# Kernel tuning notes

Hardware: AMD Instinct MI355X
Metric: run time of the kernel (lower is better)

Reference implementation:

```python
import jax, jax.numpy as jnp
import numpy as np

N, IN_F, OUT_F = 4096, 512, 256
GRAPH_DENSITY = 0.01
NEG_FILL = -1e11  # torch code uses -100000000000.0


def _normalise(g, remove_diagonal):
    # dense branch of normalise_graph (self_connection=False)
    if remove_diagonal:
        g = g - jnp.diag(jnp.diag(g))
    s = g.sum(axis=1)
    s = jnp.where(s == 0.0, 1.0, s)
    d = s ** -0.5
    return d[:, None] * g * d[None, :]


def setup_inputs() -> dict:
    key = jax.random.key(0)
    k1, k2, k3, k4, k5 = jax.random.split(key, 5)
    x = jax.random.normal(k1, (N, IN_F), jnp.float32)
    graph = (jax.random.uniform(k2, (N, N)) < GRAPH_DENSITY).astype(jnp.float32)
    # fc/weight: kaiming-normal-like init
    weight = jax.random.normal(k3, (OUT_F, IN_F), jnp.float32) * np.float32(np.sqrt(2.0 / IN_F))
    t_s = jax.random.normal(k4, (1, OUT_F), jnp.float32) * 0.05
    t_r = jax.random.normal(k5, (1, OUT_F), jnp.float32) * 0.05
    return {"x": x, "graph": graph, "weight": weight, "t_s": t_s, "t_r": t_r}


def reference(x, graph, weight, t_s, t_r):
    # H_ = input @ weight.T   (no bias, no dropout)
    H = x @ weight.T  # [N, OUT_F]

    # get_mask(graph, power=1): normalise(remove_diag) then normalise again
    mask = _normalise(_normalise(graph, remove_diagonal=True), remove_diagonal=False)  # [N, N]

    # get_edge_index_attention, dense path, attention_features == 1
    C1 = jax.nn.leaky_relu(H @ t_s.T, negative_slope=0.2)       # [N, 1]
    C2 = jax.nn.leaky_relu(H @ t_r.T, negative_slope=0.2).T    # [1, N]
    S = (mask * C1 + mask * C2) * 0.5                           # [N, N]
    S = jnp.where(mask <= 0.0, NEG_FILL, S)
    A = jax.nn.softmax(S, axis=1)                               # neighbourhood softmax

    # normalise_graph(A, remove_diagonal=False, self_connection=True), dense path
    A = A + jnp.eye(A.shape[0], dtype=A.dtype)
    s = A.sum(axis=1)
    s = jnp.where(s == 0.0, 1.0, s)
    d = s ** -0.5
    C = d[:, None] * A * d[None, :]

    return C @ H  # [N, OUT_F]
```

## Files before the change

### kernel.cpp

```cpp
#include <hip/hip_runtime.h>
#include <hip/hip_bf16.h>
#include <math.h>

#define N 4096
#define IN_F 512
#define OUT_F 256
#define CAP 128

typedef __attribute__((ext_vector_type(8))) short short8;
typedef __attribute__((ext_vector_type(4))) float float4v;

static __device__ __forceinline__ ushort f2bf(float f) {
  unsigned u = __float_as_uint(f);
  unsigned rnd = 0x7fffu + ((u >> 16) & 1u);
  return (ushort)((u + rnd) >> 16);
}

__global__ __launch_bounds__(256) void build_csr(
    const float* __restrict__ g, int* __restrict__ cols,
    int* __restrict__ deg, float* __restrict__ d1,
    float* __restrict__ c1r, float* __restrict__ c2r) {
  int i = blockIdx.x;
  __shared__ int s_cnt;
  if (threadIdx.x == 0) { s_cnt = 0; c1r[i] = 0.f; c2r[i] = 0.f; }
  __syncthreads();
  const float4* row4 = (const float4*)(g + (size_t)i * N);
  int lane = threadIdx.x & 63;
  for (int it = threadIdx.x; it < N / 4; it += 256) {
    float4 v = row4[it];
    int jb = it * 4;
    bool nz0 = (v.x != 0.f) && (jb + 0 != i);
    bool nz1 = (v.y != 0.f) && (jb + 1 != i);
    bool nz2 = (v.z != 0.f) && (jb + 2 != i);
    bool nz3 = (v.w != 0.f) && (jb + 3 != i);
    unsigned long long m0 = __ballot(nz0);
    unsigned long long m1 = __ballot(nz1);
    unsigned long long m2 = __ballot(nz2);
    unsigned long long m3 = __ballot(nz3);
    int p0 = __popcll(m0), p1 = __popcll(m1), p2 = __popcll(m2), p3 = __popcll(m3);
    int total = p0 + p1 + p2 + p3;
    if (total > 0) {
      int base;
      if (lane == 0) base = atomicAdd(&s_cnt, total);
      base = __shfl(base, 0);
      unsigned long long ltm = (1ull << lane) - 1ull;
      if (nz0) { int p = base + __popcll(m0 & ltm);                 if (p < CAP) cols[(size_t)i * CAP + p] = jb + 0; }
      if (nz1) { int p = base + p0 + __popcll(m1 & ltm);            if (p < CAP) cols[(size_t)i * CAP + p] = jb + 1; }
      if (nz2) { int p = base + p0 + p1 + __popcll(m2 & ltm);       if (p < CAP) cols[(size_t)i * CAP + p] = jb + 2; }
      if (nz3) { int p = base + p0 + p1 + p2 + __popcll(m3 & ltm);  if (p < CAP) cols[(size_t)i * CAP + p] = jb + 3; }
    }
  }
  __syncthreads();
  if (threadIdx.x == 0) {
    int c = s_cnt;
    deg[i] = (c > CAP) ? CAP : c;
    d1[i] = (c == 0) ? 1.f : rsqrtf((float)c);
  }
}

#define LDST 72
__global__ __launch_bounds__(256) void gemm_fused(
    const float* __restrict__ x, const float* __restrict__ wgt,
    const float* __restrict__ ts, const float* __restrict__ tr,
    const int* __restrict__ cols, const int* __restrict__ deg,
    const float* __restrict__ d1, float* __restrict__ w,
    float* __restrict__ H, float* __restrict__ c1r, float* __restrict__ c2r) {
  int bid = blockIdx.x;
  if (bid >= 256) {
    int i = (bid - 256) * 256 + threadIdx.x;
    int dgi = deg[i];
    float sum = 0.f;
    for (int k = 0; k < dgi; ++k) sum += d1[cols[(size_t)i * CAP + k]];
    float s2 = d1[i] * sum;
    float dd2 = (s2 == 0.f) ? 1.f : rsqrtf(s2);
    w[i] = d1[i] * dd2;
    return;
  }
  __shared__ __align__(16) ushort As[64 * LDST];
  __shared__ __align__(16) ushort Bs[64 * LDST];
  int bm = (bid >> 2) * 64;
  int bn = (bid & 3) * 64;
  int tid = threadIdx.x;
  int lane = tid & 63;
  int wv = tid >> 6;
  int wm = (wv >> 1) * 32, wn = (wv & 1) * 32;

  float4v acc[2][2] = {{{0.f,0.f,0.f,0.f},{0.f,0.f,0.f,0.f}},
                       {{0.f,0.f,0.f,0.f},{0.f,0.f,0.f,0.f}}};

  for (int k0 = 0; k0 < IN_F; k0 += 64) {
    #pragma unroll
    for (int p = 0; p < 4; ++p) {
      int idx = p * 256 + tid;
      int row = idx >> 4;
      int cg = idx & 15;
      float4 va = *(const float4*)(x   + (size_t)(bm + row) * IN_F + k0 + cg * 4);
      float4 vb = *(const float4*)(wgt + (size_t)(bn + row) * IN_F + k0 + cg * 4);
      ushort4 pa, pb;
      pa.x = f2bf(va.x); pa.y = f2bf(va.y); pa.z = f2bf(va.z); pa.w = f2bf(va.w);
      pb.x = f2bf(vb.x); pb.y = f2bf(vb.y); pb.z = f2bf(vb.z); pb.w = f2bf(vb.w);
      *(ushort4*)(As + row * LDST + cg * 4) = pa;
      *(ushort4*)(Bs + row * LDST + cg * 4) = pb;
    }
    __syncthreads();
    #pragma unroll
    for (int kk = 0; kk < 64; kk += 32) {
      int kof = kk + (lane >> 4) * 8;
      short8 a0 = *(const short8*)(As + (wm +      (lane & 15)) * LDST + kof);
      short8 a1 = *(const short8*)(As + (wm + 16 + (lane & 15)) * LDST + kof);
      short8 b0 = *(const short8*)(Bs + (wn +      (lane & 15)) * LDST + kof);
      short8 b1 = *(const short8*)(Bs + (wn + 16 + (lane & 15)) * LDST + kof);
      acc[0][0] = __builtin_amdgcn_mfma_f32_16x16x32_bf16(a0, b0, acc[0][0], 0, 0, 0);
      acc[0][1] = __builtin_amdgcn_mfma_f32_16x16x32_bf16(a0, b1, acc[0][1], 0, 0, 0);
      acc[1][0] = __builtin_amdgcn_mfma_f32_16x16x32_bf16(a1, b0, acc[1][0], 0, 0, 0);
      acc[1][1] = __builtin_amdgcn_mfma_f32_16x16x32_bf16(a1, b1, acc[1][1], 0, 0, 0);
    }
    __syncthreads();
  }
  int ccol = lane & 15;
  int crow = (lane >> 4) * 4;
  float ts0 = ts[bn + wn + ccol],      ts1 = ts[bn + wn + 16 + ccol];
  float tr0 = tr[bn + wn + ccol],      tr1 = tr[bn + wn + 16 + ccol];
  #pragma unroll
  for (int rt = 0; rt < 2; ++rt) {
    #pragma unroll
    for (int r = 0; r < 4; ++r) {
      float ps = acc[rt][0][r] * ts0 + acc[rt][1][r] * ts1;
      float pr = acc[rt][0][r] * tr0 + acc[rt][1][r] * tr1;
      #pragma unroll
      for (int off = 1; off < 16; off <<= 1) {
        ps += __shfl_xor(ps, off);
        pr += __shfl_xor(pr, off);
      }
      if (ccol == 0) {
        int row = bm + wm + rt * 16 + crow + r;
        atomicAdd(&c1r[row], ps);
        atomicAdd(&c2r[row], pr);
      }
    }
  }
  #pragma unroll
  for (int rt = 0; rt < 2; ++rt)
    #pragma unroll
    for (int ct = 0; ct < 2; ++ct)
      #pragma unroll
      for (int r = 0; r < 4; ++r) {
        int gr = bm + wm + rt * 16 + crow + r;
        int gc = bn + wn + ct * 16 + ccol;
        H[(size_t)gr * OUT_F + gc] = acc[rt][ct][r];
      }
}

__global__ __launch_bounds__(256) void aggregate(
    const float* __restrict__ H, const int* __restrict__ cols,
    const int* __restrict__ deg, const float* __restrict__ w,
    const float* __restrict__ c1r, const float* __restrict__ c2r,
    float* __restrict__ out) {
  __shared__ int sJ[4][CAP];
  __shared__ float sA[4][CAP];
  int wv = threadIdx.x >> 6;
  int lane = threadIdx.x & 63;
  int i = blockIdx.x * 4 + wv;
  int dgi = deg[i];
  float wi = w[i];
  float c1v = c1r[i];
  float ci = c1v > 0.f ? c1v : 0.2f * c1v;

  float S0 = -1e30f, S1 = -1e30f;
  int j0 = 0, j1 = 0;
  if (lane < dgi) {
    j0 = cols[(size_t)i * CAP + lane];
    float c2v = c2r[j0];
    float cj = c2v > 0.f ? c2v : 0.2f * c2v;
    S0 = 0.5f * wi * w[j0] * (ci + cj);
  }
  if (lane + 64 < dgi) {
    j1 = cols[(size_t)i * CAP + lane + 64];
    float c2v = c2r[j1];
    float cj = c2v > 0.f ? c2v : 0.2f * c2v;
    S1 = 0.5f * wi * w[j1] * (ci + cj);
  }
  float mx = fmaxf(S0, S1);
  #pragma unroll
  for (int off = 32; off > 0; off >>= 1) mx = fmaxf(mx, __shfl_xor(mx, off));
  float e0 = (lane < dgi) ? __expf(S0 - mx) : 0.f;
  float e1 = (lane + 64 < dgi) ? __expf(S1 - mx) : 0.f;
  float Z = e0 + e1;
  #pragma unroll
  for (int off = 32; off > 0; off >>= 1) Z += __shfl_xor(Z, off);
  float half_invZ = 0.5f / Z;
  if (lane < dgi)      { sJ[wv][lane] = j0;        sA[wv][lane] = e0 * half_invZ; }
  if (lane + 64 < dgi) { sJ[wv][lane + 64] = j1;   sA[wv][lane + 64] = e1 * half_invZ; }
  __syncthreads();

  float4 hself = ((const float4*)(H + (size_t)i * OUT_F))[lane];
  float4 accv;
  accv.x = 0.5f * hself.x; accv.y = 0.5f * hself.y;
  accv.z = 0.5f * hself.z; accv.w = 0.5f * hself.w;

  if (dgi > 0) {
    int k = 0;
    for (; k + 8 <= dgi; k += 8) {
      int jj[8]; float aa[8];
      #pragma unroll
      for (int u = 0; u < 8; ++u) { jj[u] = sJ[wv][k + u]; aa[u] = sA[wv][k + u]; }
      float4 h[8];
      #pragma unroll
      for (int u = 0; u < 8; ++u)
        h[u] = ((const float4*)(H + (size_t)jj[u] * OUT_F))[lane];
      #pragma unroll
      for (int u = 0; u < 8; ++u) {
        accv.x += aa[u] * h[u].x;
        accv.y += aa[u] * h[u].y;
        accv.z += aa[u] * h[u].z;
        accv.w += aa[u] * h[u].w;
      }
    }
    for (; k < dgi; ++k) {
      int ja = sJ[wv][k];
      float aa = sA[wv][k];
      float4 ha = ((const float4*)(H + (size_t)ja * OUT_F))[lane];
      accv.x += aa * ha.x; accv.y += aa * ha.y;
      accv.z += aa * ha.z; accv.w += aa * ha.w;
    }
  } else {
    float4 s = {0.f, 0.f, 0.f, 0.f};
    for (int r = 0; r < N; ++r) {
      float4 h = ((const float4*)(H + (size_t)r * OUT_F))[lane];
      s.x += h.x; s.y += h.y; s.z += h.z; s.w += h.w;
    }
    const float inv = 0.5f / (float)N;
    accv.x += s.x * inv; accv.y += s.y * inv;
    accv.z += s.z * inv; accv.w += s.w * inv;
  }
  ((float4*)(out + (size_t)i * OUT_F))[lane] = accv;
}

extern "C" void kernel_launch(void* const* d_in, const int* in_sizes, int n_in,
                              void* d_out, int out_size, void* d_ws, size_t ws_size,
                              hipStream_t stream) {
  const float* x     = (const float*)d_in[0];
  const float* graph = (const float*)d_in[1];
  const float* wgt   = (const float*)d_in[2];
  const float* ts    = (const float*)d_in[3];
  const float* tr    = (const float*)d_in[4];
  float* out = (float*)d_out;

  char* ws = (char*)d_ws;
  float* H    = (float*)(ws);
  int*   cols = (int*)  (ws + (size_t)4 * 1024 * 1024);
  int*   deg  = (int*)  (ws + (size_t)6 * 1024 * 1024);
  float* d1   = (float*)(ws + (size_t)6 * 1024 * 1024 + 16384);
  float* w    = (float*)(ws + (size_t)6 * 1024 * 1024 + 32768);
  float* c1r  = (float*)(ws + (size_t)6 * 1024 * 1024 + 49152);
  float* c2r  = (float*)(ws + (size_t)6 * 1024 * 1024 + 65536);

  build_csr<<<N, 256, 0, stream>>>(graph, cols, deg, d1, c1r, c2r);
  gemm_fused<<<272, 256, 0, stream>>>(x, wgt, ts, tr, cols, deg, d1, w, H, c1r, c2r);
  aggregate<<<N / 4, 256, 0, stream>>>(H, cols, deg, w, c1r, c2r, out);
}
```

Before: 138.6 us.

## Gather neighbour rows from a bf16 copy of H and compute C1 in aggregate

The GEMM now also writes a bf16 copy of H, and the aggregate kernel gathers neighbour rows from it, halving the bytes per gathered row. The per-row C1 score is now taken in aggregate as a dot of the row's own H with t_s, which removes the C1 atomics from the GEMM epilogue. The per-row degree normalisation is reworked from one thread per row with a serial loop into a wave-per-row reduction, using 320 blocks. A block-wide __syncthreads in aggregate is dropped because each wave only reads its own shared slots, and bf16 H lowers the precision of the aggregation.

```diff
diff --git a/kernel.cpp b/kernel.cpp
--- a/kernel.cpp
+++ b/kernel.cpp
@@ -15,14 +15,16 @@
   unsigned rnd = 0x7fffu + ((u >> 16) & 1u);
   return (ushort)((u + rnd) >> 16);
 }
+static __device__ __forceinline__ float bf2f(ushort us) {
+  return __uint_as_float(((unsigned)us) << 16);
+}
 
 __global__ __launch_bounds__(256) void build_csr(
     const float* __restrict__ g, int* __restrict__ cols,
-    int* __restrict__ deg, float* __restrict__ d1,
-    float* __restrict__ c1r, float* __restrict__ c2r) {
+    int* __restrict__ deg, float* __restrict__ d1, float* __restrict__ c2r) {
   int i = blockIdx.x;
   __shared__ int s_cnt;
-  if (threadIdx.x == 0) { s_cnt = 0; c1r[i] = 0.f; c2r[i] = 0.f; }
+  if (threadIdx.x == 0) { s_cnt = 0; c2r[i] = 0.f; }
   __syncthreads();
   const float4* row4 = (const float4*)(g + (size_t)i * N);
   int lane = threadIdx.x & 63;
@@ -61,19 +63,27 @@
 #define LDST 72
 __global__ __launch_bounds__(256) void gemm_fused(
     const float* __restrict__ x, const float* __restrict__ wgt,
-    const float* __restrict__ ts, const float* __restrict__ tr,
+    const float* __restrict__ tr,
     const int* __restrict__ cols, const int* __restrict__ deg,
     const float* __restrict__ d1, float* __restrict__ w,
-    float* __restrict__ H, float* __restrict__ c1r, float* __restrict__ c2r) {
+    float* __restrict__ H, ushort* __restrict__ Hb, float* __restrict__ c2r) {
   int bid = blockIdx.x;
   if (bid >= 256) {
-    int i = (bid - 256) * 256 + threadIdx.x;
-    int dgi = deg[i];
-    float sum = 0.f;
-    for (int k = 0; k < dgi; ++k) sum += d1[cols[(size_t)i * CAP + k]];
-    float s2 = d1[i] * sum;
-    float dd2 = (s2 == 0.f) ? 1.f : rsqrtf(s2);
-    w[i] = d1[i] * dd2;
+    int wv = threadIdx.x >> 6, lane = threadIdx.x & 63;
+    int wave_id = (bid - 256) * 4 + wv;
+    for (int r = 0; r < 16; ++r) {
+      int i = wave_id * 16 + r;
+      int dgi = deg[i];
+      float v = 0.f;
+      if (lane < dgi)      v  = d1[cols[(size_t)i * CAP + lane]];
+      if (lane + 64 < dgi) v += d1[cols[(size_t)i * CAP + lane + 64]];
+      #pragma unroll
+      for (int off = 32; off > 0; off >>= 1) v += __shfl_xor(v, off);
+      if (lane == 0) {
+        float s2 = d1[i] * v;
+        w[i] = d1[i] * ((s2 == 0.f) ? 1.f : rsqrtf(s2));
+      }
+    }
     return;
   }
   __shared__ __align__(16) ushort As[64 * LDST];
@@ -119,22 +129,16 @@
   }
   int ccol = lane & 15;
   int crow = (lane >> 4) * 4;
-  float ts0 = ts[bn + wn + ccol],      ts1 = ts[bn + wn + 16 + ccol];
-  float tr0 = tr[bn + wn + ccol],      tr1 = tr[bn + wn + 16 + ccol];
+  float tr0 = tr[bn + wn + ccol], tr1 = tr[bn + wn + 16 + ccol];
   #pragma unroll
   for (int rt = 0; rt < 2; ++rt) {
     #pragma unroll
     for (int r = 0; r < 4; ++r) {
-      float ps = acc[rt][0][r] * ts0 + acc[rt][1][r] * ts1;
       float pr = acc[rt][0][r] * tr0 + acc[rt][1][r] * tr1;
       #pragma unroll
-      for (int off = 1; off < 16; off <<= 1) {
-        ps += __shfl_xor(ps, off);
-        pr += __shfl_xor(pr, off);
-      }
+      for (int off = 1; off < 16; off <<= 1) pr += __shfl_xor(pr, off);
       if (ccol == 0) {
         int row = bm + wm + rt * 16 + crow + r;
-        atomicAdd(&c1r[row], ps);
         atomicAdd(&c2r[row], pr);
       }
     }
@@ -147,15 +151,17 @@
       for (int r = 0; r < 4; ++r) {
         int gr = bm + wm + rt * 16 + crow + r;
         int gc = bn + wn + ct * 16 + ccol;
-        H[(size_t)gr * OUT_F + gc] = acc[rt][ct][r];
+        float v = acc[rt][ct][r];
+        H[(size_t)gr * OUT_F + gc] = v;
+        Hb[(size_t)gr * OUT_F + gc] = f2bf(v);
       }
 }
 
 __global__ __launch_bounds__(256) void aggregate(
-    const float* __restrict__ H, const int* __restrict__ cols,
-    const int* __restrict__ deg, const float* __restrict__ w,
-    const float* __restrict__ c1r, const float* __restrict__ c2r,
-    float* __restrict__ out) {
+    const float* __restrict__ H, const ushort* __restrict__ Hb,
+    const int* __restrict__ cols, const int* __restrict__ deg,
+    const float* __restrict__ w, const float* __restrict__ ts,
+    const float* __restrict__ c2r, float* __restrict__ out) {
   __shared__ int sJ[4][CAP];
   __shared__ float sA[4][CAP];
   int wv = threadIdx.x >> 6;
@@ -163,8 +169,13 @@
   int i = blockIdx.x * 4 + wv;
   int dgi = deg[i];
   float wi = w[i];
-  float c1v = c1r[i];
-  float ci = c1v > 0.f ? c1v : 0.2f * c1v;
+
+  float4 hself = ((const float4*)(H + (size_t)i * OUT_F))[lane];
+  float4 t4 = ((const float4*)ts)[lane];
+  float c1 = hself.x * t4.x + hself.y * t4.y + hself.z * t4.z + hself.w * t4.w;
+  #pragma unroll
+  for (int off = 32; off > 0; off >>= 1) c1 += __shfl_xor(c1, off);
+  float ci = c1 > 0.f ? c1 : 0.2f * c1;
 
   float S0 = -1e30f, S1 = -1e30f;
   int j0 = 0, j1 = 0;
@@ -191,9 +202,7 @@
   float half_invZ = 0.5f / Z;
   if (lane < dgi)      { sJ[wv][lane] = j0;        sA[wv][lane] = e0 * half_invZ; }
   if (lane + 64 < dgi) { sJ[wv][lane + 64] = j1;   sA[wv][lane + 64] = e1 * half_invZ; }
-  __syncthreads();
-
-  float4 hself = ((const float4*)(H + (size_t)i * OUT_F))[lane];
+
   float4 accv;
   accv.x = 0.5f * hself.x; accv.y = 0.5f * hself.y;
   accv.z = 0.5f * hself.z; accv.w = 0.5f * hself.w;
@@ -204,30 +213,31 @@
       int jj[8]; float aa[8];
       #pragma unroll
       for (int u = 0; u < 8; ++u) { jj[u] = sJ[wv][k + u]; aa[u] = sA[wv][k + u]; }
-      float4 h[8];
+      ushort4 hb[8];
       #pragma unroll
       for (int u = 0; u < 8; ++u)
-        h[u] = ((const float4*)(H + (size_t)jj[u] * OUT_F))[lane];
+        hb[u] = ((const ushort4*)(Hb + (size_t)jj[u] * OUT_F))[lane];
       #pragma unroll
       for (int u = 0; u < 8; ++u) {
-        accv.x += aa[u] * h[u].x;
-        accv.y += aa[u] * h[u].y;
-        accv.z += aa[u] * h[u].z;
-        accv.w += aa[u] * h[u].w;
+        accv.x += aa[u] * bf2f(hb[u].x);
+        accv.y += aa[u] * bf2f(hb[u].y);
+        accv.z += aa[u] * bf2f(hb[u].z);
+        accv.w += aa[u] * bf2f(hb[u].w);
       }
     }
     for (; k < dgi; ++k) {
       int ja = sJ[wv][k];
       float aa = sA[wv][k];
-      float4 ha = ((const float4*)(H + (size_t)ja * OUT_F))[lane];
-      accv.x += aa * ha.x; accv.y += aa * ha.y;
-      accv.z += aa * ha.z; accv.w += aa * ha.w;
+      ushort4 hbv = ((const ushort4*)(Hb + (size_t)ja * OUT_F))[lane];
+      accv.x += aa * bf2f(hbv.x); accv.y += aa * bf2f(hbv.y);
+      accv.z += aa * bf2f(hbv.z); accv.w += aa * bf2f(hbv.w);
     }
   } else {
     float4 s = {0.f, 0.f, 0.f, 0.f};
     for (int r = 0; r < N; ++r) {
-      float4 h = ((const float4*)(H + (size_t)r * OUT_F))[lane];
-      s.x += h.x; s.y += h.y; s.z += h.z; s.w += h.w;
+      ushort4 hbv = ((const ushort4*)(Hb + (size_t)r * OUT_F))[lane];
+      s.x += bf2f(hbv.x); s.y += bf2f(hbv.y);
+      s.z += bf2f(hbv.z); s.w += bf2f(hbv.w);
     }
     const float inv = 0.5f / (float)N;
     accv.x += s.x * inv; accv.y += s.y * inv;
@@ -247,15 +257,15 @@
   float* out = (float*)d_out;
 
   char* ws = (char*)d_ws;
-  float* H    = (float*)(ws);
-  int*   cols = (int*)  (ws + (size_t)4 * 1024 * 1024);
-  int*   deg  = (int*)  (ws + (size_t)6 * 1024 * 1024);
-  float* d1   = (float*)(ws + (size_t)6 * 1024 * 1024 + 16384);
-  float* w    = (float*)(ws + (size_t)6 * 1024 * 1024 + 32768);
-  float* c1r  = (float*)(ws + (size_t)6 * 1024 * 1024 + 49152);
-  float* c2r  = (float*)(ws + (size_t)6 * 1024 * 1024 + 65536);
-
-  build_csr<<<N, 256, 0, stream>>>(graph, cols, deg, d1, c1r, c2r);
-  gemm_fused<<<272, 256, 0, stream>>>(x, wgt, ts, tr, cols, deg, d1, w, H, c1r, c2r);
-  aggregate<<<N / 4, 256, 0, stream>>>(H, cols, deg, w, c1r, c2r, out);
-}
+  float*  H    = (float*) (ws);
+  ushort* Hb   = (ushort*)(ws + (size_t)4 * 1024 * 1024);
+  int*    cols = (int*)   (ws + (size_t)6 * 1024 * 1024);
+  int*    deg  = (int*)   (ws + (size_t)8 * 1024 * 1024);
+  float*  d1   = (float*) (ws + (size_t)8 * 1024 * 1024 + 16384);
+  float*  w    = (float*) (ws + (size_t)8 * 1024 * 1024 + 32768);
+  float*  c2r  = (float*) (ws + (size_t)8 * 1024 * 1024 + 49152);
+
+  build_csr<<<N, 256, 0, stream>>>(graph, cols, deg, d1, c2r);
+  gemm_fused<<<320, 256, 0, stream>>>(x, wgt, tr, cols, deg, d1, w, H, Hb, c2r);
+  aggregate<<<N / 4, 256, 0, stream>>>(H, Hb, cols, deg, w, ts, c2r, out);
+}
```

Result: faster. 135.3 us (-2.4%).
